# Kernel tuning notes

Hardware: AMD Instinct MI355X
Metric: run time of the kernel (lower is better)

## Reference

```python
import jax, jax.numpy as jnp
import numpy as np

K = 16        # top-K nodes per sample (from self.K)
C_IN = 2048   # conv1 in_channels
C_OUT = 256   # conv1 out_channels
D_OUT = 512   # fc1 out_features (in_features = K*C_OUT = 4096)


def setup_inputs() -> dict:
    key = jax.random.key(0)
    k0, k1, k2 = jax.random.split(key, 3)
    N, W, H = 128, 16, 16
    sounds = jax.random.normal(k0, (N, C_IN, W, H), dtype=jnp.float32)
    conv_w = jax.random.normal(k1, (C_OUT, C_IN), dtype=jnp.float32) * 0.02
    conv_b = jnp.zeros((C_OUT,), jnp.float32)
    fc_w = jax.random.normal(k2, (D_OUT, K * C_OUT), dtype=jnp.float32) * 0.02
    fc_b = jnp.zeros((D_OUT,), jnp.float32)
    return {"sounds": sounds, "conv_w": conv_w, "conv_b": conv_b,
            "fc_w": fc_w, "fc_b": fc_b}


def _dynamic_lnorm(rows, cols):
    """Symmetric-normalized spatial-affinity graph over the K nodes.

    Reconstructs the (undefined) Graph_Init.Dynamic_Lnorm: adjacency from
    spatial proximity of node coordinates, D^{-1/2} A D^{-1/2}.
    rows, cols: [N, K] int -> Lnorm [N, K, K] float.
    """
    coords = jnp.stack([rows, cols], axis=-1).astype(jnp.float32)  # [N,K,2]
    d2 = jnp.sum((coords[:, :, None, :] - coords[:, None, :, :]) ** 2, axis=-1)
    A = jnp.exp(-d2 / (2.0 * K))          # soft adjacency, self-loop weight 1
    dinv = jax.lax.rsqrt(jnp.sum(A, axis=-1))
    return A * dinv[:, :, None] * dinv[:, None, :]


def reference(sounds, conv_w, conv_b, fc_w, fc_b):
    N, C, W, H = sounds.shape
    # channel-sum saliency map (the original adds all channels into Fre)
    fre = jnp.sum(sounds, axis=1)                       # [N, W, H]
    feat = fre.reshape(N, W * H)
    _, idx = jax.lax.top_k(feat, K)                     # [N, K] descending (== sort[:, :K])
    # faithful replication of the original (off-by-one) coordinate math
    rows = jnp.where(idx < H, idx // H, idx // H - 1)   # [N, K]
    cols = jnp.where(idx % H == 0, H - 1, idx % H - 1)  # [N, K]
    # gather node features: [N, K, C]
    nodes = sounds[jnp.arange(N)[:, None], :, rows, cols]
    lnorm = _dynamic_lnorm(rows, cols)                  # [N, K, K]
    # conv1x1 on [K, C, 1, 1] == per-node linear 2048 -> 256, then ReLU
    x = jax.nn.relu(jnp.einsum('nkc,oc->nko', nodes, conv_w) + conv_b)  # [N,K,256]
    # graph aggregation: Lnorm @ x per sample
    y = jnp.einsum('nij,njo->nio', lnorm, x)            # [N, K, 256]
    # flatten nodes and apply fc1 (4096 -> 512)
    return y.reshape(N, K * C_OUT) @ fc_w.T + fc_b      # [N, 512]
```

## Files before the change

kernel.cpp:

```cpp
#include <hip/hip_runtime.h>
#include <math.h>

#define NB   128
#define CIN  2048
#define PP   256
#define KK   16
#define CO   256
#define DO   512

#define WS_PARTIAL 0
#define WS_POS     1048576
#define WS_LNORM   1050624
#define WS_NODEST  1083392
#define WS_XPART   5277696
#define WS_Y       6326272

__global__ __launch_bounds__(256) void k_init(float* __restrict__ out,
                                              const float* __restrict__ fcb) {
    int i = blockIdx.x * 256 + threadIdx.x;
    out[i] = fcb[i & 511];
}

__global__ __launch_bounds__(256) void k_reduce(const float* __restrict__ snd,
                                                float* __restrict__ partial) {
    int n = blockIdx.x, chunk = blockIdx.y, t = threadIdx.x;
    int sub = t >> 6, p4 = t & 63;
    const float4* base = (const float4*)(snd + (size_t)n * CIN * PP
                                         + (size_t)(chunk * 256 + sub * 64) * PP) + p4;
    float4 acc = make_float4(0.f, 0.f, 0.f, 0.f);
#pragma unroll 4
    for (int c = 0; c < 64; ++c) {
        float4 v = base[c * 64];
        acc.x += v.x; acc.y += v.y; acc.z += v.z; acc.w += v.w;
    }
    ((float4*)(partial + (size_t)(n * 32 + chunk * 4 + sub) * 256))[p4] = acc;
}

__global__ __launch_bounds__(256) void k_topk_lnorm(const float* __restrict__ partial,
                                                    int* __restrict__ pos,
                                                    float* __restrict__ lnorm) {
    int n = blockIdx.x, t = threadIdx.x;
    int lane = t & 63, wv = t >> 6;
    __shared__ float wval[4];
    __shared__ int   widx[4];
    __shared__ int   sel[16];
    __shared__ float rr[16], cc[16], dinv[16];
    __shared__ float Ash[256];

    float v = 0.f;
#pragma unroll 8
    for (int j = 0; j < 32; ++j) v += partial[(size_t)(n * 32 + j) * 256 + t];

    for (int k = 0; k < 16; ++k) {
        float bv = v; int bi = t;
#pragma unroll
        for (int off = 32; off > 0; off >>= 1) {
            float ov = __shfl_xor(bv, off, 64);
            int   oi = __shfl_xor(bi, off, 64);
            if (ov > bv || (ov == bv && oi < bi)) { bv = ov; bi = oi; }
        }
        if (lane == 0) { wval[wv] = bv; widx[wv] = bi; }
        __syncthreads();
        float best = wval[0]; int besti = widx[0];
#pragma unroll
        for (int w = 1; w < 4; ++w) {
            float ww = wval[w]; int wi = widx[w];
            if (ww > best || (ww == best && wi < besti)) { best = ww; besti = wi; }
        }
        if (t == besti) v = -INFINITY;
        if (t == 0) sel[k] = besti;
        __syncthreads();
    }

    if (t < 16) {
        int idx = sel[t];
        int r = (idx < 16) ? (idx >> 4) : ((idx >> 4) - 1);
        int c = ((idx & 15) == 0) ? 15 : ((idx & 15) - 1);
        pos[n * 16 + t] = r * 16 + c;
        rr[t] = (float)r; cc[t] = (float)c;
    }
    __syncthreads();
    {
        int i = t >> 4, j = t & 15;
        float dr = rr[i] - rr[j], dc = cc[i] - cc[j];
        Ash[t] = expf(-(dr * dr + dc * dc) * (1.0f / 32.0f));
    }
    __syncthreads();
    if (t < 16) {
        float srow = 0.f;
#pragma unroll
        for (int j = 0; j < 16; ++j) srow += Ash[t * 16 + j];
        dinv[t] = rsqrtf(srow);
    }
    __syncthreads();
    {
        int i = t >> 4, j = t & 15;
        lnorm[(size_t)n * 256 + t] = Ash[t] * dinv[i] * dinv[j];
    }
}

__global__ __launch_bounds__(256) void k_gather(const float* __restrict__ snd,
                                                const int* __restrict__ pos,
                                                float* __restrict__ nodesT) {
    int n = blockIdx.x, cb = blockIdx.y, t = threadIdx.x;
    __shared__ int lpos[16];
    if (t < 16) lpos[t] = pos[n * 16 + t];
    __syncthreads();
    int k = t & 15, cl = t >> 4;
    int p = lpos[k];
    const float* base = snd + (size_t)n * CIN * PP;
#pragma unroll
    for (int it = 0; it < 16; ++it) {
        int c = cb * 256 + it * 16 + cl;
        nodesT[(size_t)c * 2048 + n * 16 + k] = base[(size_t)c * PP + p];
    }
}

__global__ __launch_bounds__(256) void k_conv(const float* __restrict__ At,
                                              const float* __restrict__ W,
                                              float* __restrict__ Xpart) {
    int bm = blockIdx.x, bo = blockIdx.y, kc = blockIdx.z, t = threadIdx.x;
    int to = t & 15, tm = t >> 4;
    __shared__ float As[16][64];
    __shared__ float Bs[16 * 68];
    float acc[4][4] = {};
    int m0 = bm * 64, o0 = bo * 64;
    for (int c0 = kc * 1024; c0 < kc * 1024 + 1024; c0 += 16) {
#pragma unroll
        for (int i = 0; i < 4; ++i) {
            int e = i * 256 + t;
            int k = e >> 6, m = e & 63;
            As[k][m] = At[(size_t)(c0 + k) * 2048 + m0 + m];
        }
#pragma unroll
        for (int i = 0; i < 4; ++i) {
            int e = i * 256 + t;
            int o = e >> 4, k = e & 15;
            Bs[k * 68 + o] = W[(size_t)(o0 + o) * 2048 + c0 + k];
        }
        __syncthreads();
#pragma unroll
        for (int k = 0; k < 16; ++k) {
            float4 a = *(const float4*)&As[k][tm * 4];
            float4 b = *(const float4*)&Bs[k * 68 + to * 4];
            acc[0][0] += a.x * b.x; acc[0][1] += a.x * b.y; acc[0][2] += a.x * b.z; acc[0][3] += a.x * b.w;
            acc[1][0] += a.y * b.x; acc[1][1] += a.y * b.y; acc[1][2] += a.y * b.z; acc[1][3] += a.y * b.w;
            acc[2][0] += a.z * b.x; acc[2][1] += a.z * b.y; acc[2][2] += a.z * b.z; acc[2][3] += a.z * b.w;
            acc[3][0] += a.w * b.x; acc[3][1] += a.w * b.y; acc[3][2] += a.w * b.z; acc[3][3] += a.w * b.w;
        }
        __syncthreads();
    }
    float* Xp = Xpart + (size_t)kc * 524288;
#pragma unroll
    for (int i = 0; i < 4; ++i) {
        int m = m0 + tm * 4 + i;
        *(float4*)&Xp[(size_t)m * 256 + o0 + to * 4] =
            make_float4(acc[i][0], acc[i][1], acc[i][2], acc[i][3]);
    }
}

__global__ __launch_bounds__(256) void k_xmix(const float* __restrict__ Xpart,
                                              const float* __restrict__ bias,
                                              const float* __restrict__ lnorm,
                                              float* __restrict__ Y) {
    int n = blockIdx.x, o = threadIdx.x;
    __shared__ float ln[256];
    ln[o] = lnorm[(size_t)n * 256 + o];
    float b = bias[o];
    __syncthreads();
    float xv[16];
#pragma unroll
    for (int j = 0; j < 16; ++j) {
        size_t off = (size_t)(n * 16 + j) * 256 + o;
        xv[j] = fmaxf(Xpart[off] + Xpart[524288 + off] + b, 0.0f);
    }
#pragma unroll
    for (int i = 0; i < 16; ++i) {
        float a = 0.f;
#pragma unroll
        for (int j = 0; j < 16; ++j) a += ln[i * 16 + j] * xv[j];
        Y[(size_t)n * 4096 + i * 256 + o] = a;
    }
}

__global__ __launch_bounds__(256) void k_fc(const float* __restrict__ Y,
                                            const float* __restrict__ Fw,
                                            float* __restrict__ out) {
    int bn = blockIdx.x, bd = blockIdx.y, bk = blockIdx.z, t = threadIdx.x;
    int to = t & 15, tm = t >> 4;
    __shared__ float Ys[16 * 34];
    __shared__ float Fs[16 * 68];
    float acc[2][4] = {};
    int n0 = bn * 32, d0 = bd * 64, kbase = bk * 512;
    for (int c0 = kbase; c0 < kbase + 512; c0 += 16) {
#pragma unroll
        for (int i = 0; i < 2; ++i) {
            int e = i * 256 + t;
            int m = e >> 4, k = e & 15;
            Ys[k * 34 + m] = Y[(size_t)(n0 + m) * 4096 + c0 + k];
        }
#pragma unroll
        for (int i = 0; i < 4; ++i) {
            int e = i * 256 + t;
            int d = e >> 4, k = e & 15;
            Fs[k * 68 + d] = Fw[(size_t)(d0 + d) * 4096 + c0 + k];
        }
        __syncthreads();
#pragma unroll
        for (int k = 0; k < 16; ++k) {
            float2 a = *(const float2*)&Ys[k * 34 + tm * 2];
            float4 b = *(const float4*)&Fs[k * 68 + to * 4];
            acc[0][0] += a.x * b.x; acc[0][1] += a.x * b.y;
            acc[0][2] += a.x * b.z; acc[0][3] += a.x * b.w;
            acc[1][0] += a.y * b.x; acc[1][1] += a.y * b.y;
            acc[1][2] += a.y * b.z; acc[1][3] += a.y * b.w;
        }
        __syncthreads();
    }
#pragma unroll
    for (int i = 0; i < 2; ++i) {
        int nn = n0 + tm * 2 + i;
#pragma unroll
        for (int j = 0; j < 4; ++j) {
            int d = d0 + to * 4 + j;
            atomicAdd(&out[(size_t)nn * 512 + d], acc[i][j]);
        }
    }
}

extern "C" void kernel_launch(void* const* d_in, const int* in_sizes, int n_in,
                              void* d_out, int out_size, void* d_ws, size_t ws_size,
                              hipStream_t stream) {
    const float* snd    = (const float*)d_in[0];
    const float* conv_w = (const float*)d_in[1];
    const float* conv_b = (const float*)d_in[2];
    const float* fc_w   = (const float*)d_in[3];
    const float* fc_b   = (const float*)d_in[4];
    float* out = (float*)d_out;
    float* ws  = (float*)d_ws;

    float* partial = ws + WS_PARTIAL;
    int*   pos     = (int*)(ws + WS_POS);
    float* lnorm   = ws + WS_LNORM;
    float* nodesT  = ws + WS_NODEST;
    float* Xpart   = ws + WS_XPART;
    float* Y       = ws + WS_Y;

    k_init<<<256, 256, 0, stream>>>(out, fc_b);
    k_reduce<<<dim3(128, 8), 256, 0, stream>>>(snd, partial);
    k_topk_lnorm<<<128, 256, 0, stream>>>(partial, pos, lnorm);
    k_gather<<<dim3(128, 8), 256, 0, stream>>>(snd, pos, nodesT);
    k_conv<<<dim3(32, 4, 2), 256, 0, stream>>>(nodesT, conv_w, Xpart);
    k_xmix<<<128, 256, 0, stream>>>(Xpart, conv_b, lnorm, Y);
    k_fc<<<dim3(4, 8, 8), 256, 0, stream>>>(Y, fc_w, out);
}
```

Before: 538.3 us.

## Use bf16 MFMA for conv1x1 GEMM with bf16 node gather and weights

Converts the gathered node features and conv weights to bf16. The node features are now stored in row-major [N*K, C] layout, and the weights are converted in a prep kernel that is merged with the output-bias init. The conv GEMM now uses mfma_f32_16x16x32_bf16 instead of scalar fp32 FMAs. This aims to cut the conv compute time and halve its memory traffic, at the cost of bf16 rounding on the inputs to the matmul. The dominant cost is still the full reduction over the sounds tensor, so the overall gain is bounded.

```diff
diff --git a/kernel.cpp b/kernel.cpp
--- a/kernel.cpp
+++ b/kernel.cpp
@@ -1,5 +1,10 @@
 #include <hip/hip_runtime.h>
 #include <math.h>
+
+typedef __attribute__((ext_vector_type(8))) short short8;
+typedef __attribute__((ext_vector_type(4))) float f32x4;
+typedef unsigned short ushort;
+typedef unsigned int uint;
 
 #define NB   128
 #define CIN  2048
@@ -11,14 +16,33 @@
 #define WS_PARTIAL 0
 #define WS_POS     1048576
 #define WS_LNORM   1050624
-#define WS_NODEST  1083392
-#define WS_XPART   5277696
-#define WS_Y       6326272
-
-__global__ __launch_bounds__(256) void k_init(float* __restrict__ out,
-                                              const float* __restrict__ fcb) {
-    int i = blockIdx.x * 256 + threadIdx.x;
-    out[i] = fcb[i & 511];
+#define WS_NODES   1083392
+#define WS_WB      3180544
+#define WS_XPART   3442688
+#define WS_Y       4491264
+
+__device__ __forceinline__ ushort f2bf(float f) {
+    uint u = __builtin_bit_cast(uint, f);
+    u += 0x7fffu + ((u >> 16) & 1u);
+    return (ushort)(u >> 16);
+}
+
+__global__ __launch_bounds__(256) void k_prep(const float* __restrict__ conv_w,
+                                              ushort* __restrict__ Wb,
+                                              const float* __restrict__ fcb,
+                                              float* __restrict__ out) {
+    int b = blockIdx.x, t = threadIdx.x;
+    if (b < 512) {
+        int idx = (b * 256 + t) * 4;
+        float4 v = *(const float4*)(conv_w + idx);
+        uint2 u;
+        u.x = (uint)f2bf(v.x) | ((uint)f2bf(v.y) << 16);
+        u.y = (uint)f2bf(v.z) | ((uint)f2bf(v.w) << 16);
+        *(uint2*)(Wb + idx) = u;
+    } else {
+        int i = (b - 512) * 256 + t;
+        out[i] = fcb[i & 511];
+    }
 }
 
 __global__ __launch_bounds__(256) void k_reduce(const float* __restrict__ snd,
@@ -101,61 +125,65 @@
 
 __global__ __launch_bounds__(256) void k_gather(const float* __restrict__ snd,
                                                 const int* __restrict__ pos,
-                                                float* __restrict__ nodesT) {
+                                                ushort* __restrict__ nodes) {
     int n = blockIdx.x, cb = blockIdx.y, t = threadIdx.x;
     __shared__ int lpos[16];
     if (t < 16) lpos[t] = pos[n * 16 + t];
     __syncthreads();
-    int k = t & 15, cl = t >> 4;
+    int k = t & 15, ci = t >> 4;
     int p = lpos[k];
-    const float* base = snd + (size_t)n * CIN * PP;
-#pragma unroll
-    for (int it = 0; it < 16; ++it) {
-        int c = cb * 256 + it * 16 + cl;
-        nodesT[(size_t)c * 2048 + n * 16 + k] = base[(size_t)c * PP + p];
-    }
-}
-
-__global__ __launch_bounds__(256) void k_conv(const float* __restrict__ At,
-                                              const float* __restrict__ W,
+    const float* base = snd + (size_t)n * CIN * PP + (size_t)(cb * 128 + ci * 8) * PP + p;
+    uint q[4];
+#pragma unroll
+    for (int i = 0; i < 4; ++i) {
+        ushort a = f2bf(base[(size_t)(2 * i) * PP]);
+        ushort b = f2bf(base[(size_t)(2 * i + 1) * PP]);
+        q[i] = (uint)a | ((uint)b << 16);
+    }
+    uint4 qq = make_uint4(q[0], q[1], q[2], q[3]);
+    *(uint4*)(nodes + (size_t)(n * 16 + k) * 2048 + cb * 128 + ci * 8) = qq;
+}
+
+__global__ __launch_bounds__(256) void k_conv(const ushort* __restrict__ nodes,
+                                              const ushort* __restrict__ Wb,
                                               float* __restrict__ Xpart) {
     int bm = blockIdx.x, bo = blockIdx.y, kc = blockIdx.z, t = threadIdx.x;
-    int to = t & 15, tm = t >> 4;
-    __shared__ float As[16][64];
-    __shared__ float Bs[16 * 68];
-    float acc[4][4] = {};
+    int w = t >> 6, l = t & 63;
+    int lm = l & 15, quad = l >> 4;
+    __shared__ ushort As[64 * 40];
+    __shared__ ushort Bs[64 * 40];
+    f32x4 acc[4] = {{0.f,0.f,0.f,0.f},{0.f,0.f,0.f,0.f},{0.f,0.f,0.f,0.f},{0.f,0.f,0.f,0.f}};
     int m0 = bm * 64, o0 = bo * 64;
-    for (int c0 = kc * 1024; c0 < kc * 1024 + 1024; c0 += 16) {
-#pragma unroll
-        for (int i = 0; i < 4; ++i) {
-            int e = i * 256 + t;
-            int k = e >> 6, m = e & 63;
-            As[k][m] = At[(size_t)(c0 + k) * 2048 + m0 + m];
-        }
-#pragma unroll
-        for (int i = 0; i < 4; ++i) {
-            int e = i * 256 + t;
-            int o = e >> 4, k = e & 15;
-            Bs[k * 68 + o] = W[(size_t)(o0 + o) * 2048 + c0 + k];
-        }
-        __syncthreads();
-#pragma unroll
-        for (int k = 0; k < 16; ++k) {
-            float4 a = *(const float4*)&As[k][tm * 4];
-            float4 b = *(const float4*)&Bs[k * 68 + to * 4];
-            acc[0][0] += a.x * b.x; acc[0][1] += a.x * b.y; acc[0][2] += a.x * b.z; acc[0][3] += a.x * b.w;
-            acc[1][0] += a.y * b.x; acc[1][1] += a.y * b.y; acc[1][2] += a.y * b.z; acc[1][3] += a.y * b.w;
-            acc[2][0] += a.z * b.x; acc[2][1] += a.z * b.y; acc[2][2] += a.z * b.z; acc[2][3] += a.z * b.w;
-            acc[3][0] += a.w * b.x; acc[3][1] += a.w * b.y; acc[3][2] += a.w * b.z; acc[3][3] += a.w * b.w;
-        }
-        __syncthreads();
-    }
+    int row = t >> 2, seg = t & 3;
+    const ushort* asrc = nodes + (size_t)(m0 + row) * 2048 + seg * 8;
+    const ushort* bsrc = Wb + (size_t)(o0 + row) * 2048 + seg * 8;
+    uint4* adst = (uint4*)(As + row * 40 + seg * 8);
+    uint4* bdst = (uint4*)(Bs + row * 40 + seg * 8);
+    const ushort* ard = As + (w * 16 + lm) * 40 + quad * 8;
+    const ushort* brd = Bs + lm * 40 + quad * 8;
+
+    for (int c0 = kc * 1024; c0 < kc * 1024 + 1024; c0 += 32) {
+        *adst = *(const uint4*)(asrc + c0);
+        *bdst = *(const uint4*)(bsrc + c0);
+        __syncthreads();
+        short8 af = *(const short8*)ard;
+#pragma unroll
+        for (int ot = 0; ot < 4; ++ot) {
+            short8 bf = *(const short8*)(brd + ot * 16 * 40);
+            acc[ot] = __builtin_amdgcn_mfma_f32_16x16x32_bf16(af, bf, acc[ot], 0, 0, 0);
+        }
+        __syncthreads();
+    }
+
     float* Xp = Xpart + (size_t)kc * 524288;
 #pragma unroll
-    for (int i = 0; i < 4; ++i) {
-        int m = m0 + tm * 4 + i;
-        *(float4*)&Xp[(size_t)m * 256 + o0 + to * 4] =
-            make_float4(acc[i][0], acc[i][1], acc[i][2], acc[i][3]);
+    for (int ot = 0; ot < 4; ++ot) {
+        int o = o0 + ot * 16 + lm;
+#pragma unroll
+        for (int r = 0; r < 4; ++r) {
+            int m = m0 + w * 16 + quad * 4 + r;
+            Xp[(size_t)m * 256 + o] = acc[ot][r];
+        }
     }
 }
 
@@ -239,18 +267,19 @@
     float* out = (float*)d_out;
     float* ws  = (float*)d_ws;
 
-    float* partial = ws + WS_PARTIAL;
-    int*   pos     = (int*)(ws + WS_POS);
-    float* lnorm   = ws + WS_LNORM;
-    float* nodesT  = ws + WS_NODEST;
-    float* Xpart   = ws + WS_XPART;
-    float* Y       = ws + WS_Y;
-
-    k_init<<<256, 256, 0, stream>>>(out, fc_b);
+    float*  partial = ws + WS_PARTIAL;
+    int*    pos     = (int*)(ws + WS_POS);
+    float*  lnorm   = ws + WS_LNORM;
+    ushort* nodes   = (ushort*)(ws + WS_NODES);
+    ushort* Wb      = (ushort*)(ws + WS_WB);
+    float*  Xpart   = ws + WS_XPART;
+    float*  Y       = ws + WS_Y;
+
+    k_prep<<<768, 256, 0, stream>>>(conv_w, Wb, fc_b, out);
     k_reduce<<<dim3(128, 8), 256, 0, stream>>>(snd, partial);
     k_topk_lnorm<<<128, 256, 0, stream>>>(partial, pos, lnorm);
-    k_gather<<<dim3(128, 8), 256, 0, stream>>>(snd, pos, nodesT);
-    k_conv<<<dim3(32, 4, 2), 256, 0, stream>>>(nodesT, conv_w, Xpart);
+    k_gather<<<dim3(128, 16), 256, 0, stream>>>(snd, pos, nodes);
+    k_conv<<<dim3(32, 4, 2), 256, 0, stream>>>(nodes, Wb, Xpart);
     k_xmix<<<128, 256, 0, stream>>>(Xpart, conv_b, lnorm, Y);
     k_fc<<<dim3(4, 8, 8), 256, 0, stream>>>(Y, fc_w, out);
 }
```

After: 487.5 us. 1.1x faster.
